# Kernel optimization log

Measured on AMD Instinct MI355X. Metric: run time of the kernel, lower is better.

The kernel has to match this reference:

```python
import jax, jax.numpy as jnp
import numpy as np

N_SERIES = 32768
N_TIME = 512
SEAS = 24
MAX_NUM_SERIES = 32768
OUTPUT_SIZE = 7


def setup_inputs() -> dict:
    key = jax.random.key(0)
    k1, k2, k3, k4, k5 = jax.random.split(key, 5)
    # y must be strictly positive (divisions and logs of levels)
    y = jax.random.uniform(k1, (N_SERIES, N_TIME), jnp.float32) + 0.5
    idxs = jax.random.randint(k2, (N_SERIES,), 0, MAX_NUM_SERIES)
    lev_sms = jax.random.normal(k3, (MAX_NUM_SERIES, 1), jnp.float32) * 0.5
    seas_sms = jax.random.normal(k4, (MAX_NUM_SERIES, 1), jnp.float32) * 0.5
    init_seas = jax.random.normal(k5, (MAX_NUM_SERIES, SEAS), jnp.float32) * 0.1
    return {
        "y": y,
        "idxs": idxs,
        "lev_sms": lev_sms,
        "seas_sms": seas_sms,
        "init_seas": init_seas,
        "seasonality": SEAS,
        "output_size": OUTPUT_SIZE,
    }


def _es_forward(y, idxs, lev_sms_p, seas_sms_p, init_seas_p, seasonality, output_size):
    n_series, n_time = y.shape
    lev_sms = jax.nn.sigmoid(lev_sms_p[idxs, 0])          # (n,)
    # NOTE: faithful to original code, which (buggy or not) derives seas_sms
    # from self.lev_sms as well; seas_sms_p is an unused parameter.
    seas_sms = jax.nn.sigmoid(lev_sms_p[idxs, 0])         # (n,)
    init_seas = jnp.exp(init_seas_p[idxs, :])             # (n, seasonality)

    lev0 = y[:, 0] / init_seas[:, 0]                      # levels[:,0]

    # Ring-buffer formulation of the lag-`seasonality` recurrence:
    # original reads seasonalities[:, t] and writes seasonalities[:, t+seasonality];
    # both map to slot t % seasonality (read-before-write). Initial buffer slots
    # equal init_seas columns (slot 0 = init_seas[:,0], which also covers the
    # duplicated entry seasonalities[:, seasonality]).
    positions = jnp.arange(1, n_time) % seasonality       # (n_time-1,)
    y_steps = y[:, 1:].T                                  # (n_time-1, n)

    def step(carry, xs):
        lev_prev, buf = carry                             # (n,), (n, seasonality)
        y_t, pos = xs
        seas_t = buf[:, pos]
        newlev = lev_sms * (y_t / seas_t) + (1.0 - lev_sms) * lev_prev
        newseason = seas_sms * (y_t / newlev) + (1.0 - seas_sms) * seas_t
        log_diff = jnp.log(newlev) - jnp.log(lev_prev)
        buf = buf.at[:, pos].set(newseason)
        return (newlev, buf), (newlev, newseason, log_diff)

    _, (levs, seasons, logd) = jax.lax.scan(step, (lev0, init_seas), (y_steps, positions))

    levels = jnp.concatenate([lev0[:, None], levs.T], axis=1)              # (n, n_time)
    seasonalities = jnp.concatenate(
        [init_seas, init_seas[:, :1], seasons.T], axis=1                   # (n, seasonality+n_time)
    )
    log_diff_of_levels = logd.T                                            # (n, n_time-1)

    if output_size > seasonality:
        # faithful to original (which uses len(seasonalities) == n_series)
        start = seasonalities.shape[0] - seasonality
        end = start + output_size - seasonality
        seasonalities = jnp.concatenate([seasonalities, seasonalities[:, start:end]], axis=1)

    return levels, seasonalities, log_diff_of_levels


def reference(y, idxs, lev_sms, seas_sms, init_seas, seasonality, output_size):
    return _es_forward(y, idxs, lev_sms, seas_sms, init_seas, seasonality, output_size)
```

## Files before the change

kernel.cpp:

```cpp
#include <hip/hip_runtime.h>

#define NT 512
#define SEASN 24
#define TT 64
#define YS 65

constexpr int SEA_STRIDE = NT + SEASN;
constexpr int LOG_STRIDE = NT - 1;
constexpr float LN2 = 0.6931471805599453f;

__device__ __forceinline__ float frcp(float x)  { return __builtin_amdgcn_rcpf(x); }
__device__ __forceinline__ float flog2(float x) { return __builtin_amdgcn_logf(x); }

__device__ __forceinline__ void gl_lds4(const float* g, float* lds) {
    __builtin_amdgcn_global_load_lds(
        (const __attribute__((address_space(1))) void*)g,
        (__attribute__((address_space(3))) void*)lds, 4, 0, 0);
}

template<int PHASE, bool FIRST>
__device__ __forceinline__ void compute_tile(const float* __restrict__ yb,
                                             float* __restrict__ lt,
                                             float* __restrict__ st,
                                             float* __restrict__ dt,
                                             float lsm, float (&buf)[SEASN],
                                             float& lev, float& l2p)
{
    #pragma unroll
    for (int k = 0; k < TT; ++k) {
        const int pos = (PHASE + k) % SEASN;
        const float yt = yb[k];
        if (FIRST && k == 0) {
            lev = yt * frcp(buf[0]);
            l2p = flog2(lev);
            lt[0] = lev;
            st[0] = buf[0];
        } else {
            const float sv = buf[pos];
            const float nl = lev + lsm * (yt * frcp(sv) - lev);
            const float ns = sv + lsm * (yt * frcp(nl) - sv);
            const float l2 = flog2(nl);
            lt[k] = nl; st[k] = ns; dt[k] = (l2 - l2p) * LN2;
            l2p = l2; lev = nl; buf[pos] = ns;
        }
    }
}

template<bool FIRSTTILE>
__device__ __forceinline__ void flush_tile(const float* __restrict__ lt,
                                           const float* __restrict__ st,
                                           const float* __restrict__ dt,
                                           int q, int rr, int sbase, int tbase,
                                           float* __restrict__ levels,
                                           float* __restrict__ seasv,
                                           float* __restrict__ logd)
{
    #pragma unroll
    for (int i = 0; i < 16; ++i) {
        const int r = 4 * i + rr;
        const size_t srow = (size_t)(sbase + r);
        const int off = r * YS + 4 * q;
        float4 lv = make_float4(lt[off], lt[off+1], lt[off+2], lt[off+3]);
        float4 sv = make_float4(st[off], st[off+1], st[off+2], st[off+3]);
        *(float4*)(levels + srow * NT + tbase + 4 * q) = lv;
        *(float4*)(seasv + srow * SEA_STRIDE + SEASN + tbase + 4 * q) = sv;
        float* dp = logd + srow * LOG_STRIDE + tbase + 4 * q - 1;
        if (FIRSTTILE && q == 0) {
            dp[1] = dt[off+1]; dp[2] = dt[off+2]; dp[3] = dt[off+3];
        } else {
            dp[0] = dt[off]; dp[1] = dt[off+1]; dp[2] = dt[off+2]; dp[3] = dt[off+3];
        }
    }
}

__global__ __launch_bounds__(64)
void es_fwd(const float* __restrict__ y, const int* __restrict__ idxs,
            const float* __restrict__ lev_sms_p, const float* __restrict__ init_seas_p,
            float* __restrict__ levels, float* __restrict__ seasv,
            float* __restrict__ logd)
{
    __shared__ float ybuf [64 * YS];
    __shared__ float ltile[64 * YS];
    __shared__ float stile[64 * YS];
    __shared__ float dtile[64 * YS];

    const int lane  = threadIdx.x;
    const int sbase = blockIdx.x * 64;
    const int q  = lane & 15;
    const int rr = lane >> 4;

    auto stage = [&](int m) {
        const float* g = y + (size_t)sbase * NT + m * TT + lane;
        #pragma unroll
        for (int r = 0; r < 64; ++r)
            gl_lds4(g + (size_t)r * NT, &ybuf[r * YS]);
    };

    stage(0);

    const int idx = idxs[sbase + lane];
    const float lsm = frcp(1.0f + __expf(-lev_sms_p[idx]));

    float buf[SEASN];
    {
        const float4* is4 = (const float4*)(init_seas_p + (size_t)idx * SEASN);
        #pragma unroll
        for (int g = 0; g < 6; ++g) {
            float4 v = is4[g];
            buf[4*g+0] = __expf(v.x); buf[4*g+1] = __expf(v.y);
            buf[4*g+2] = __expf(v.z); buf[4*g+3] = __expf(v.w);
            #pragma unroll
            for (int j = 0; j < 4; ++j)
                ltile[lane * YS + 4*g + j] = buf[4*g+j];
        }
    }

    if (q < 6) {
        #pragma unroll
        for (int i = 0; i < 16; ++i) {
            const int r = 4 * i + rr;
            const size_t srow = (size_t)(sbase + r);
            const int off = r * YS + 4 * q;
            float4 v = make_float4(ltile[off], ltile[off+1], ltile[off+2], ltile[off+3]);
            *(float4*)(seasv + srow * SEA_STRIDE + 4 * q) = v;
        }
    }

    float lev, l2p;
    const float* yb = &ybuf[lane * YS];
    float* lt = &ltile[lane * YS];
    float* st = &stile[lane * YS];
    float* dt = &dtile[lane * YS];

    __builtin_amdgcn_s_waitcnt(0);
    compute_tile<0, true >(yb, lt, st, dt, lsm, buf, lev, l2p);
    stage(1);
    flush_tile<true >(ltile, stile, dtile, q, rr, sbase, 0 * TT, levels, seasv, logd);
    __builtin_amdgcn_s_waitcnt(0);

#define TILE(M, PHASE, LAST) \
    compute_tile<PHASE, false>(yb, lt, st, dt, lsm, buf, lev, l2p); \
    if (!(LAST)) stage((M) + 1); \
    flush_tile<false>(ltile, stile, dtile, q, rr, sbase, (M) * TT, levels, seasv, logd); \
    if (!(LAST)) __builtin_amdgcn_s_waitcnt(0);

    TILE(1, 16, false)
    TILE(2,  8, false)
    TILE(3,  0, false)
    TILE(4, 16, false)
    TILE(5,  8, false)
    TILE(6,  0, false)
    TILE(7, 16, true)
#undef TILE
}

extern "C" void kernel_launch(void* const* d_in, const int* in_sizes, int n_in,
                              void* d_out, int out_size, void* d_ws, size_t ws_size,
                              hipStream_t stream)
{
    const float* y         = (const float*)d_in[0];
    const int*   idxs      = (const int*)d_in[1];
    const float* lev_sms   = (const float*)d_in[2];
    const float* init_seas = (const float*)d_in[4];
    const int n_series = in_sizes[1];

    float* levels = (float*)d_out;
    float* seasv  = levels + (size_t)n_series * NT;
    float* logdv  = seasv  + (size_t)n_series * SEA_STRIDE;

    es_fwd<<<n_series / 64, 64, 0, stream>>>(y, idxs, lev_sms, init_seas,
                                             levels, seasv, logdv);
}
```

Measured before the change: 337.9 us.

## Split recurrence and memory traffic into producer/consumer waves with double buffering

Each block now runs two wavefronts. Wave 0 runs the serial recurrence over 32-step subtiles into double-buffered LDS. Wave 1 stages y tiles into LDS, writes the previous subtile's outputs to global memory, and computes the log-differences there, moving that work off the critical serial path. The goal is to overlap the latency-bound recurrence with global loads and stores. The cost is a barrier every subtile and twice the threads per block.

```diff
diff --git a/kernel.cpp b/kernel.cpp
--- a/kernel.cpp
+++ b/kernel.cpp
@@ -2,12 +2,13 @@
 
 #define NT 512
 #define SEASN 24
-#define TT 64
-#define YS 65
 
 constexpr int SEA_STRIDE = NT + SEASN;
 constexpr int LOG_STRIDE = NT - 1;
 constexpr float LN2 = 0.6931471805599453f;
+
+constexpr int YS = 65;
+constexpr int TS = 33;
 
 __device__ __forceinline__ float frcp(float x)  { return __builtin_amdgcn_rcpf(x); }
 __device__ __forceinline__ float flog2(float x) { return __builtin_amdgcn_logf(x); }
@@ -19,139 +20,148 @@
 }
 
 template<int PHASE, bool FIRST>
-__device__ __forceinline__ void compute_tile(const float* __restrict__ yb,
-                                             float* __restrict__ lt,
-                                             float* __restrict__ st,
-                                             float* __restrict__ dt,
-                                             float lsm, float (&buf)[SEASN],
-                                             float& lev, float& l2p)
+__device__ __forceinline__ void compute_subtile(const float* __restrict__ yb,
+                                                float* __restrict__ lt,
+                                                float* __restrict__ st,
+                                                float lsm, float (&buf)[SEASN],
+                                                float& lev)
 {
+    float yp[32];
     #pragma unroll
-    for (int k = 0; k < TT; ++k) {
+    for (int k = 0; k < 32; ++k) yp[k] = yb[k];
+    #pragma unroll
+    for (int k = 0; k < 32; ++k) {
         const int pos = (PHASE + k) % SEASN;
-        const float yt = yb[k];
+        const float yt = yp[k];
         if (FIRST && k == 0) {
             lev = yt * frcp(buf[0]);
-            l2p = flog2(lev);
             lt[0] = lev;
             st[0] = buf[0];
         } else {
             const float sv = buf[pos];
             const float nl = lev + lsm * (yt * frcp(sv) - lev);
             const float ns = sv + lsm * (yt * frcp(nl) - sv);
-            const float l2 = flog2(nl);
-            lt[k] = nl; st[k] = ns; dt[k] = (l2 - l2p) * LN2;
-            l2p = l2; lev = nl; buf[pos] = ns;
+            lt[k] = nl; st[k] = ns;
+            lev = nl; buf[pos] = ns;
         }
     }
 }
 
-template<bool FIRSTTILE>
-__device__ __forceinline__ void flush_tile(const float* __restrict__ lt,
-                                           const float* __restrict__ st,
-                                           const float* __restrict__ dt,
-                                           int q, int rr, int sbase, int tbase,
-                                           float* __restrict__ levels,
-                                           float* __restrict__ seasv,
-                                           float* __restrict__ logd)
+__device__ __forceinline__ void flush_sub(const float* __restrict__ lt,
+                                          const float* __restrict__ st,
+                                          int sf, int q, int rr, int sbase,
+                                          float* __restrict__ levels,
+                                          float* __restrict__ seasv,
+                                          float* __restrict__ logd)
 {
+    const int tb = sf * 32;
     #pragma unroll
-    for (int i = 0; i < 16; ++i) {
-        const int r = 4 * i + rr;
+    for (int i = 0; i < 8; ++i) {
+        const int r = 8 * i + rr;
         const size_t srow = (size_t)(sbase + r);
-        const int off = r * YS + 4 * q;
-        float4 lv = make_float4(lt[off], lt[off+1], lt[off+2], lt[off+3]);
-        float4 sv = make_float4(st[off], st[off+1], st[off+2], st[off+3]);
-        *(float4*)(levels + srow * NT + tbase + 4 * q) = lv;
-        *(float4*)(seasv + srow * SEA_STRIDE + SEASN + tbase + 4 * q) = sv;
-        float* dp = logd + srow * LOG_STRIDE + tbase + 4 * q - 1;
-        if (FIRSTTILE && q == 0) {
-            dp[1] = dt[off+1]; dp[2] = dt[off+2]; dp[3] = dt[off+3];
-        } else {
-            dp[0] = dt[off]; dp[1] = dt[off+1]; dp[2] = dt[off+2]; dp[3] = dt[off+3];
-        }
+        const int off = r * TS + 4 * q;
+        const float l0 = lt[off], l1 = lt[off+1], l2 = lt[off+2], l3 = lt[off+3];
+        const float s0 = st[off], s1 = st[off+1], s2 = st[off+2], s3 = st[off+3];
+        *(float4*)(levels + srow * NT + tb + 4*q)                  = make_float4(l0,l1,l2,l3);
+        *(float4*)(seasv  + srow * SEA_STRIDE + SEASN + tb + 4*q)  = make_float4(s0,s1,s2,s3);
+        const float lm1 = (q == 0) ? lt[r * TS + 32] : lt[off - 1];
+        const float g0 = flog2(lm1), g1 = flog2(l0), g2 = flog2(l1),
+                    g3 = flog2(l2),  g4 = flog2(l3);
+        float* dp = logd + srow * LOG_STRIDE + tb + 4*q - 1;
+        if (!(sf == 0 && q == 0)) dp[0] = (g1 - g0) * LN2;
+        dp[1] = (g2 - g1) * LN2;
+        dp[2] = (g3 - g2) * LN2;
+        dp[3] = (g4 - g3) * LN2;
     }
 }
 
-__global__ __launch_bounds__(64)
+__global__ __launch_bounds__(128)
 void es_fwd(const float* __restrict__ y, const int* __restrict__ idxs,
             const float* __restrict__ lev_sms_p, const float* __restrict__ init_seas_p,
             float* __restrict__ levels, float* __restrict__ seasv,
             float* __restrict__ logd)
 {
-    __shared__ float ybuf [64 * YS];
-    __shared__ float ltile[64 * YS];
-    __shared__ float stile[64 * YS];
-    __shared__ float dtile[64 * YS];
+    __shared__ float ybuf[2][64 * YS];
+    __shared__ float ltb [2][64 * TS];
+    __shared__ float stb [2][64 * TS];
 
-    const int lane  = threadIdx.x;
+    const int tid   = threadIdx.x;
+    const int wid   = tid >> 6;
+    const int lane  = tid & 63;
     const int sbase = blockIdx.x * 64;
-    const int q  = lane & 15;
-    const int rr = lane >> 4;
+    const int q  = lane & 7;
+    const int rr = lane >> 3;
 
-    auto stage = [&](int m) {
-        const float* g = y + (size_t)sbase * NT + m * TT + lane;
+    auto stage = [&](int T) {
+        const float* g = y + (size_t)sbase * NT + T * 64 + lane;
+        float* l = ybuf[T & 1];
         #pragma unroll
         for (int r = 0; r < 64; ++r)
-            gl_lds4(g + (size_t)r * NT, &ybuf[r * YS]);
+            gl_lds4(g + (size_t)r * NT, l + r * YS);
     };
 
-    stage(0);
+    float buf[SEASN];
+    float lsm = 0.0f;
+    float lev = 1.0f;
 
-    const int idx = idxs[sbase + lane];
-    const float lsm = frcp(1.0f + __expf(-lev_sms_p[idx]));
-
-    float buf[SEASN];
-    {
+    if (wid == 0) {
+        const int idx = idxs[sbase + lane];
+        lsm = frcp(1.0f + __expf(-lev_sms_p[idx]));
         const float4* is4 = (const float4*)(init_seas_p + (size_t)idx * SEASN);
         #pragma unroll
-        for (int g = 0; g < 6; ++g) {
-            float4 v = is4[g];
-            buf[4*g+0] = __expf(v.x); buf[4*g+1] = __expf(v.y);
-            buf[4*g+2] = __expf(v.z); buf[4*g+3] = __expf(v.w);
-            #pragma unroll
-            for (int j = 0; j < 4; ++j)
-                ltile[lane * YS + 4*g + j] = buf[4*g+j];
+        for (int g4i = 0; g4i < 6; ++g4i) {
+            float4 v = is4[g4i];
+            buf[4*g4i+0] = __expf(v.x); buf[4*g4i+1] = __expf(v.y);
+            buf[4*g4i+2] = __expf(v.z); buf[4*g4i+3] = __expf(v.w);
         }
+        #pragma unroll
+        for (int j = 0; j < SEASN; ++j)
+            ltb[1][lane * TS + j] = buf[j];
+        asm volatile("s_waitcnt lgkmcnt(0)" ::: "memory");
+    } else {
+        stage(0);
+        asm volatile("s_waitcnt vmcnt(0)" ::: "memory");
     }
+    __builtin_amdgcn_s_barrier();
+    asm volatile("" ::: "memory");
 
-    if (q < 6) {
-        #pragma unroll
-        for (int i = 0; i < 16; ++i) {
-            const int r = 4 * i + rr;
-            const size_t srow = (size_t)(sbase + r);
-            const int off = r * YS + 4 * q;
-            float4 v = make_float4(ltile[off], ltile[off+1], ltile[off+2], ltile[off+3]);
-            *(float4*)(seasv + srow * SEA_STRIDE + 4 * q) = v;
+    for (int s = 0; s < 16; ++s) {
+        if (wid == 0) {
+            const float* yb = &ybuf[(s >> 1) & 1][lane * YS + (s & 1) * 32];
+            float* lt = &ltb[s & 1][lane * TS];
+            float* st = &stb[s & 1][lane * TS];
+            lt[32] = lev;
+            const int ph = s % 3;
+            if (s == 0)       compute_subtile<0,  true >(yb, lt, st, lsm, buf, lev);
+            else if (ph == 0) compute_subtile<0,  false>(yb, lt, st, lsm, buf, lev);
+            else if (ph == 1) compute_subtile<8,  false>(yb, lt, st, lsm, buf, lev);
+            else              compute_subtile<16, false>(yb, lt, st, lsm, buf, lev);
+            asm volatile("s_waitcnt lgkmcnt(0)" ::: "memory");
+        } else {
+            const int T = (s >> 1) + 1;
+            if (!(s & 1) && T < 8) stage(T);
+            if (s == 0) {
+                if (q < 6) {
+                    #pragma unroll
+                    for (int i = 0; i < 8; ++i) {
+                        const int r = 8 * i + rr;
+                        const int off = r * TS + 4 * q;
+                        float4 v = make_float4(ltb[1][off],   ltb[1][off+1],
+                                               ltb[1][off+2], ltb[1][off+3]);
+                        *(float4*)(seasv + (size_t)(sbase + r) * SEA_STRIDE + 4 * q) = v;
+                    }
+                }
+            } else {
+                flush_sub(ltb[(s-1)&1], stb[(s-1)&1], s-1, q, rr, sbase,
+                          levels, seasv, logd);
+            }
+            asm volatile("s_waitcnt vmcnt(48)" ::: "memory");
         }
+        __builtin_amdgcn_s_barrier();
+        asm volatile("" ::: "memory");
     }
-
-    float lev, l2p;
-    const float* yb = &ybuf[lane * YS];
-    float* lt = &ltile[lane * YS];
-    float* st = &stile[lane * YS];
-    float* dt = &dtile[lane * YS];
-
-    __builtin_amdgcn_s_waitcnt(0);
-    compute_tile<0, true >(yb, lt, st, dt, lsm, buf, lev, l2p);
-    stage(1);
-    flush_tile<true >(ltile, stile, dtile, q, rr, sbase, 0 * TT, levels, seasv, logd);
-    __builtin_amdgcn_s_waitcnt(0);
-
-#define TILE(M, PHASE, LAST) \
-    compute_tile<PHASE, false>(yb, lt, st, dt, lsm, buf, lev, l2p); \
-    if (!(LAST)) stage((M) + 1); \
-    flush_tile<false>(ltile, stile, dtile, q, rr, sbase, (M) * TT, levels, seasv, logd); \
-    if (!(LAST)) __builtin_amdgcn_s_waitcnt(0);
-
-    TILE(1, 16, false)
-    TILE(2,  8, false)
-    TILE(3,  0, false)
-    TILE(4, 16, false)
-    TILE(5,  8, false)
-    TILE(6,  0, false)
-    TILE(7, 16, true)
-#undef TILE
+    if (wid == 1)
+        flush_sub(ltb[1], stb[1], 15, q, rr, sbase, levels, seasv, logd);
 }
 
 extern "C" void kernel_launch(void* const* d_in, const int* in_sizes, int n_in,
@@ -168,6 +178,6 @@
     float* seasv  = levels + (size_t)n_series * NT;
     float* logdv  = seasv  + (size_t)n_series * SEA_STRIDE;
 
-    es_fwd<<<n_series / 64, 64, 0, stream>>>(y, idxs, lev_sms, init_seas,
-                                             levels, seasv, logdv);
+    es_fwd<<<n_series / 64, 128, 0, stream>>>(y, idxs, lev_sms, init_seas,
+                                              levels, seasv, logdv);
 }
```

After: 329.3 us. 2.5% less time.

## Parallelize recurrence within each season window via affine scan across lanes

Applied to the files above, without the earlier changes.

Replaces the one-thread-per-series sequential recurrence with 32-lane groups per series. Within each 24-step seasonal window the level recurrence is linear (affine), so it is computed with a warp shuffle prefix scan and the seasonal updates are applied in parallel. This removes the serial dependency chain and the LDS staging tiles. In exchange it adds shuffle overhead, uses 24 of 32 lanes, and issues narrow per-lane global loads and stores instead of staged float4 writes. The reassociated arithmetic may also change floating-point rounding.

```diff
diff --git a/kernel.cpp b/kernel.cpp
--- a/kernel.cpp
+++ b/kernel.cpp
@@ -2,8 +2,6 @@
 
 #define NT 512
 #define SEASN 24
-#define TT 64
-#define YS 65
 
 constexpr int SEA_STRIDE = NT + SEASN;
 constexpr int LOG_STRIDE = NT - 1;
@@ -12,146 +10,79 @@
 __device__ __forceinline__ float frcp(float x)  { return __builtin_amdgcn_rcpf(x); }
 __device__ __forceinline__ float flog2(float x) { return __builtin_amdgcn_logf(x); }
 
-__device__ __forceinline__ void gl_lds4(const float* g, float* lds) {
-    __builtin_amdgcn_global_load_lds(
-        (const __attribute__((address_space(1))) void*)g,
-        (__attribute__((address_space(3))) void*)lds, 4, 0, 0);
-}
-
-template<int PHASE, bool FIRST>
-__device__ __forceinline__ void compute_tile(const float* __restrict__ yb,
-                                             float* __restrict__ lt,
-                                             float* __restrict__ st,
-                                             float* __restrict__ dt,
-                                             float lsm, float (&buf)[SEASN],
-                                             float& lev, float& l2p)
-{
-    #pragma unroll
-    for (int k = 0; k < TT; ++k) {
-        const int pos = (PHASE + k) % SEASN;
-        const float yt = yb[k];
-        if (FIRST && k == 0) {
-            lev = yt * frcp(buf[0]);
-            l2p = flog2(lev);
-            lt[0] = lev;
-            st[0] = buf[0];
-        } else {
-            const float sv = buf[pos];
-            const float nl = lev + lsm * (yt * frcp(sv) - lev);
-            const float ns = sv + lsm * (yt * frcp(nl) - sv);
-            const float l2 = flog2(nl);
-            lt[k] = nl; st[k] = ns; dt[k] = (l2 - l2p) * LN2;
-            l2p = l2; lev = nl; buf[pos] = ns;
-        }
-    }
-}
-
-template<bool FIRSTTILE>
-__device__ __forceinline__ void flush_tile(const float* __restrict__ lt,
-                                           const float* __restrict__ st,
-                                           const float* __restrict__ dt,
-                                           int q, int rr, int sbase, int tbase,
-                                           float* __restrict__ levels,
-                                           float* __restrict__ seasv,
-                                           float* __restrict__ logd)
-{
-    #pragma unroll
-    for (int i = 0; i < 16; ++i) {
-        const int r = 4 * i + rr;
-        const size_t srow = (size_t)(sbase + r);
-        const int off = r * YS + 4 * q;
-        float4 lv = make_float4(lt[off], lt[off+1], lt[off+2], lt[off+3]);
-        float4 sv = make_float4(st[off], st[off+1], st[off+2], st[off+3]);
-        *(float4*)(levels + srow * NT + tbase + 4 * q) = lv;
-        *(float4*)(seasv + srow * SEA_STRIDE + SEASN + tbase + 4 * q) = sv;
-        float* dp = logd + srow * LOG_STRIDE + tbase + 4 * q - 1;
-        if (FIRSTTILE && q == 0) {
-            dp[1] = dt[off+1]; dp[2] = dt[off+2]; dp[3] = dt[off+3];
-        } else {
-            dp[0] = dt[off]; dp[1] = dt[off+1]; dp[2] = dt[off+2]; dp[3] = dt[off+3];
-        }
-    }
-}
-
-__global__ __launch_bounds__(64)
+__global__ __launch_bounds__(256)
 void es_fwd(const float* __restrict__ y, const int* __restrict__ idxs,
             const float* __restrict__ lev_sms_p, const float* __restrict__ init_seas_p,
             float* __restrict__ levels, float* __restrict__ seasv,
             float* __restrict__ logd)
 {
-    __shared__ float ybuf [64 * YS];
-    __shared__ float ltile[64 * YS];
-    __shared__ float stile[64 * YS];
-    __shared__ float dtile[64 * YS];
+    const int tid  = threadIdx.x;
+    const int lane = tid & 63;
+    const int li   = lane & 31;
+    const int g    = lane >> 5;
+    const int wv   = tid >> 6;
+    const int srow = blockIdx.x * 8 + wv * 2 + g;
 
-    const int lane  = threadIdx.x;
-    const int sbase = blockIdx.x * 64;
-    const int q  = lane & 15;
-    const int rr = lane >> 4;
+    const size_t yrow = (size_t)srow * NT;
+    const int idx = idxs[srow];
+    const float a = frcp(1.0f + __expf(-lev_sms_p[idx]));
+    const float A = 1.0f - a;
 
-    auto stage = [&](int m) {
-        const float* g = y + (size_t)sbase * NT + m * TT + lane;
-        #pragma unroll
-        for (int r = 0; r < 64; ++r)
-            gl_lds4(g + (size_t)r * NT, &ybuf[r * YS]);
-    };
+    const int p = (1 + li) % SEASN;
+    float sreg = 1.0f;
+    if (li < 24) sreg = __expf(init_seas_p[(size_t)idx * SEASN + p]);
 
-    stage(0);
+    const float is0 = init_seas_p[(size_t)idx * SEASN];
+    float lev  = y[yrow] * frcp(__expf(is0));
+    float glev = flog2(lev);
 
-    const int idx = idxs[sbase + lane];
-    const float lsm = frcp(1.0f + __expf(-lev_sms_p[idx]));
+    float* lrow = levels + (size_t)srow * NT;
+    float* vrow = seasv  + (size_t)srow * SEA_STRIDE;
+    float* drow = logd   + (size_t)srow * LOG_STRIDE;
 
-    float buf[SEASN];
-    {
-        const float4* is4 = (const float4*)(init_seas_p + (size_t)idx * SEASN);
-        #pragma unroll
-        for (int g = 0; g < 6; ++g) {
-            float4 v = is4[g];
-            buf[4*g+0] = __expf(v.x); buf[4*g+1] = __expf(v.y);
-            buf[4*g+2] = __expf(v.z); buf[4*g+3] = __expf(v.w);
-            #pragma unroll
-            for (int j = 0; j < 4; ++j)
-                ltile[lane * YS + 4*g + j] = buf[4*g+j];
-        }
+    if (li == 0) lrow[0] = lev;
+    if (li < 24) {
+        vrow[p] = sreg;
+        if (li == 23) vrow[24] = sreg;
     }
 
-    if (q < 6) {
+    float ycur = (li < 24) ? y[yrow + 1 + li] : 1.0f;
+
+    for (int w = 0; w < 22; ++w) {
+        const int W = (w < 21) ? 24 : 7;
+
+        float ynext = 1.0f;
+        if (w < 21) {
+            const int Wn = (w + 1 < 21) ? 24 : 7;
+            if (li < Wn) ynext = y[yrow + 1 + 24 * (w + 1) + li];
+        }
+
+        const float c = a * ycur * frcp(sreg);
+
+        float P = A, Q = c;
         #pragma unroll
-        for (int i = 0; i < 16; ++i) {
-            const int r = 4 * i + rr;
-            const size_t srow = (size_t)(sbase + r);
-            const int off = r * YS + 4 * q;
-            float4 v = make_float4(ltile[off], ltile[off+1], ltile[off+2], ltile[off+3]);
-            *(float4*)(seasv + srow * SEA_STRIDE + 4 * q) = v;
+        for (int d = 1; d < 32; d <<= 1) {
+            const float Pp = __shfl(P, lane - d);
+            const float Qp = __shfl(Q, lane - d);
+            if (li >= d) { Q += P * Qp; P *= Pp; }
         }
+        const float nl = P * lev + Q;
+        const float ns = a * ycur * frcp(nl) + A * sreg;
+        const float gv = flog2(nl);
+        const float gsh = __shfl(gv, lane - 1);
+        const float gp  = (li == 0) ? glev : gsh;
+
+        if (li < W) {
+            const int t = 1 + 24 * w + li;
+            lrow[t]      = nl;
+            vrow[t + 24] = ns;
+            drow[t - 1]  = (gv - gp) * LN2;
+            sreg = ns;
+        }
+        lev  = __shfl(nl, (g << 5) + (W - 1));
+        glev = __shfl(gv, (g << 5) + (W - 1));
+        ycur = ynext;
     }
-
-    float lev, l2p;
-    const float* yb = &ybuf[lane * YS];
-    float* lt = &ltile[lane * YS];
-    float* st = &stile[lane * YS];
-    float* dt = &dtile[lane * YS];
-
-    __builtin_amdgcn_s_waitcnt(0);
-    compute_tile<0, true >(yb, lt, st, dt, lsm, buf, lev, l2p);
-    stage(1);
-    flush_tile<true >(ltile, stile, dtile, q, rr, sbase, 0 * TT, levels, seasv, logd);
-    __builtin_amdgcn_s_waitcnt(0);
-
-#define TILE(M, PHASE, LAST) \
-    compute_tile<PHASE, false>(yb, lt, st, dt, lsm, buf, lev, l2p); \
-    if (!(LAST)) stage((M) + 1); \
-    flush_tile<false>(ltile, stile, dtile, q, rr, sbase, (M) * TT, levels, seasv, logd); \
-    if (!(LAST)) __builtin_amdgcn_s_waitcnt(0);
-
-    TILE(1, 16, false)
-    TILE(2,  8, false)
-    TILE(3,  0, false)
-    TILE(4, 16, false)
-    TILE(5,  8, false)
-    TILE(6,  0, false)
-    TILE(7, 16, true)
-#undef TILE
 }
 
 extern "C" void kernel_launch(void* const* d_in, const int* in_sizes, int n_in,
@@ -168,6 +99,6 @@
     float* seasv  = levels + (size_t)n_series * NT;
     float* logdv  = seasv  + (size_t)n_series * SEA_STRIDE;
 
-    es_fwd<<<n_series / 64, 64, 0, stream>>>(y, idxs, lev_sms, init_seas,
+    es_fwd<<<n_series / 8, 256, 0, stream>>>(y, idxs, lev_sms, init_seas,
                                              levels, seasv, logdv);
 }
```

Result: no change. 337.8 us (-0.0%).
